# Performance work log

Measured on AMD Instinct MI355X. Metric: run time of the kernel, lower is better.

Reference implementation:

```python
import jax, jax.numpy as jnp
import numpy as np

D = 128      # hidden_dim
NH = 4       # nhead
FF = 64      # dim_feedforward
P = 16       # patch size
C, H, W = 3, 224, 224
NA = 15      # n_actions
BS = 256
NP = (H // P) * (W // P)      # 196 patches
PD = C * P * P                # 768 patch_dim


def _ln(x, s, b):
    m = jnp.mean(x, -1, keepdims=True)
    v = jnp.mean(jnp.square(x - m), -1, keepdims=True)
    return (x - m) / jnp.sqrt(v + 1e-5) * s + b


def _mha(q, k, v, Wqkv, bqkv, Wo, bo):
    # q,k,v: (L, B, D); Wqkv: (D, 3D) jax-layout; torch MultiheadAttention math
    Wq, Wk, Wv = jnp.split(Wqkv, 3, axis=1)
    bq, bk, bv = jnp.split(bqkv, 3)
    hd = D // NH
    Lq, B, _ = q.shape
    Lk = k.shape[0]
    Q = (q @ Wq + bq).reshape(Lq, B, NH, hd)
    K = (k @ Wk + bk).reshape(Lk, B, NH, hd)
    V = (v @ Wv + bv).reshape(Lk, B, NH, hd)
    scores = jnp.einsum('qbhd,kbhd->bhqk', Q, K) * np.float32(1.0 / np.sqrt(hd))
    attn = jax.nn.softmax(scores, axis=-1)
    out = jnp.einsum('bhqk,kbhd->qbhd', attn, V).reshape(Lq, B, D)
    return out @ Wo + bo


def setup_inputs() -> dict:
    key = jax.random.key(0)
    ks = iter(jax.random.split(key, 64))
    n = lambda shape, sc=0.02: (jax.random.normal(next(ks), shape, jnp.float32) * sc)
    inp = {
        'image': jax.random.normal(next(ks), (BS, C, H, W), jnp.float32),
        'angle': jax.random.normal(next(ks), (BS,), jnp.float32),
        'pos_x': jax.random.normal(next(ks), (BS,), jnp.float32),
        'pos_y': jax.random.normal(next(ks), (BS,), jnp.float32),
        'sk': jax.random.normal(next(ks), (BS, 200), jnp.float32),
        'patch_W': n((PD, D)), 'patch_b': n((D,)),
        'pos_emb': n((NP, 1, D), 1.0),
        'enc_qkv_W': n((D, 3 * D)), 'enc_qkv_b': n((3 * D,)),
        'enc_out_W': n((D, D)), 'enc_out_b': n((D,)),
        'enc_ln1_s': jnp.ones((D,)), 'enc_ln1_b': jnp.zeros((D,)),
        'enc_ff1_W': n((D, FF)), 'enc_ff1_b': n((FF,)),
        'enc_ff2_W': n((FF, D)), 'enc_ff2_b': n((D,)),
        'enc_ln2_s': jnp.ones((D,)), 'enc_ln2_b': jnp.zeros((D,)),
        'dec_sa_qkv_W': n((D, 3 * D)), 'dec_sa_qkv_b': n((3 * D,)),
        'dec_sa_out_W': n((D, D)), 'dec_sa_out_b': n((D,)),
        'dec_ca_qkv_W': n((D, 3 * D)), 'dec_ca_qkv_b': n((3 * D,)),
        'dec_ca_out_W': n((D, D)), 'dec_ca_out_b': n((D,)),
        'dec_ln1_s': jnp.ones((D,)), 'dec_ln1_b': jnp.zeros((D,)),
        'dec_ln2_s': jnp.ones((D,)), 'dec_ln2_b': jnp.zeros((D,)),
        'dec_ln3_s': jnp.ones((D,)), 'dec_ln3_b': jnp.zeros((D,)),
        'dec_ff1_W': n((D, FF)), 'dec_ff1_b': n((FF,)),
        'dec_ff2_W': n((FF, D)), 'dec_ff2_b': n((D,)),
        'dec_norm_s': jnp.ones((D,)), 'dec_norm_b': jnp.zeros((D,)),
        'sk1_W': n((200, 256)), 'sk1_b': n((256,)),
        'sk2_W': n((256, 256)), 'sk2_b': n((256,)),
        'sk3_W': n((256, 100)), 'sk3_b': n((100,)),
        'act_W': n((NA + 103, D)), 'act_b': n((D,)),
        'l1_W': n((D, D)), 'l1_b': n((D,)),
        'l2_W': n((D, 1)), 'l2_b': n((1,)),
    }
    return inp


def reference(image, angle, pos_x, pos_y, sk,
              patch_W, patch_b, pos_emb,
              enc_qkv_W, enc_qkv_b, enc_out_W, enc_out_b,
              enc_ln1_s, enc_ln1_b, enc_ff1_W, enc_ff1_b, enc_ff2_W, enc_ff2_b,
              enc_ln2_s, enc_ln2_b,
              dec_sa_qkv_W, dec_sa_qkv_b, dec_sa_out_W, dec_sa_out_b,
              dec_ca_qkv_W, dec_ca_qkv_b, dec_ca_out_W, dec_ca_out_b,
              dec_ln1_s, dec_ln1_b, dec_ln2_s, dec_ln2_b, dec_ln3_s, dec_ln3_b,
              dec_ff1_W, dec_ff1_b, dec_ff2_W, dec_ff2_b,
              dec_norm_s, dec_norm_b,
              sk1_W, sk1_b, sk2_W, sk2_b, sk3_W, sk3_b,
              act_W, act_b, l1_W, l1_b, l2_W, l2_b):
    b = image.shape[0]
    hh, ww = H // P, W // P
    # rearrange 'b c (h p1) (w p2) -> b (h w) (p1 p2 c)'
    x = image.reshape(b, C, hh, P, ww, P).transpose(0, 2, 4, 3, 5, 1).reshape(b, hh * ww, PD)
    src = (x @ patch_W + patch_b).transpose(1, 0, 2) + pos_emb  # (n, b, D)
    # encoder layer (post-norm, dropout=eval)
    s2 = _mha(src, src, src, enc_qkv_W, enc_qkv_b, enc_out_W, enc_out_b)
    src = _ln(src + s2, enc_ln1_s, enc_ln1_b)
    ff = jax.nn.relu(src @ enc_ff1_W + enc_ff1_b) @ enc_ff2_W + enc_ff2_b
    memory = _ln(src + ff, enc_ln2_s, enc_ln2_b)
    # sketch MLP
    s = jax.nn.relu(sk @ sk1_W + sk1_b)
    s = jax.nn.relu(s @ sk2_W + sk2_b)
    s = s @ sk3_W + sk3_b  # (b, 100)
    pos_ang = jnp.stack([angle, pos_x, pos_y], axis=1)  # (b, 3)
    # batched action encoding (replaces python double loop)
    nA = NA
    eye = jnp.broadcast_to(jnp.eye(nA, dtype=image.dtype)[None], (b, nA, nA))
    feats = jnp.concatenate([
        eye,
        jnp.broadcast_to(pos_ang[:, None, :], (b, nA, 3)),
        jnp.broadcast_to(s[:, None, :], (b, nA, 100)),
    ], axis=-1)  # (b, nA, nA+103)
    tgt = (feats @ act_W + act_b).transpose(1, 0, 2)  # (nA, b, D)
    # decoder layer (post-norm)
    t2 = _mha(tgt, tgt, tgt, dec_sa_qkv_W, dec_sa_qkv_b, dec_sa_out_W, dec_sa_out_b)
    tgt = _ln(tgt + t2, dec_ln1_s, dec_ln1_b)
    t2 = _mha(tgt, memory, memory, dec_ca_qkv_W, dec_ca_qkv_b, dec_ca_out_W, dec_ca_out_b)
    tgt = _ln(tgt + t2, dec_ln2_s, dec_ln2_b)
    ff = jax.nn.relu(tgt @ dec_ff1_W + dec_ff1_b) @ dec_ff2_W + dec_ff2_b
    tgt = _ln(tgt + ff, dec_ln3_s, dec_ln3_b)
    out = _ln(tgt, dec_norm_s, dec_norm_b)  # (nA, b, D)
    out = out.transpose(1, 0, 2)  # (b, nA, D)
    q = jax.nn.relu(out @ l1_W + l1_b) @ l2_W + l2_b  # (b, nA, 1)
    return q[..., 0]  # (b, nA)
```

## Files before the change

### kernel.cpp

```cpp
#include <hip/hip_runtime.h>
#include <math.h>

#define BSZ 256
#define DIM 128
#define NHD 4
#define NPATCH 196
#define NACT 15

typedef float f32x4 __attribute__((ext_vector_type(4)));
typedef __bf16 bf16x8 __attribute__((ext_vector_type(8)));
typedef short short8 __attribute__((ext_vector_type(8)));

__device__ __forceinline__ float wred_sum(float v) {
#pragma unroll
    for (int m = 1; m < 64; m <<= 1) v += __shfl_xor(v, m, 64);
    return v;
}
__device__ __forceinline__ float wred_max(float v) {
#pragma unroll
    for (int m = 1; m < 64; m <<= 1) v = fmaxf(v, __shfl_xor(v, m, 64));
    return v;
}
__device__ __forceinline__ ushort f2bf(float f) {
    unsigned u = __float_as_uint(f);
    return (ushort)((u + 0x7fffu + ((u >> 16) & 1u)) >> 16);
}

__global__ __launch_bounds__(256) void k_wconv(
    const float* __restrict__ pW, const float* __restrict__ qkvW,
    const float* __restrict__ outW, const float* __restrict__ ff1W,
    const float* __restrict__ ff2W, const float* __restrict__ ckvW,
    ushort* __restrict__ o)
{
    int i = blockIdx.x * 256 + threadIdx.x;
    if (i < 98304) {
        int n = i / 768, kp = i % 768;
        int c = kp >> 8, q = kp & 255;
        o[i] = f2bf(pW[(q * 3 + c) * 128 + n]); return;
    }
    i -= 98304;
    if (i < 49152) { int n = i >> 7, k = i & 127; o[98304 + i] = f2bf(qkvW[k * 384 + n]); return; }
    i -= 49152;
    if (i < 16384) { int n = i >> 7, k = i & 127; o[147456 + i] = f2bf(outW[k * 128 + n]); return; }
    i -= 16384;
    if (i < 8192)  { int n = i >> 7, k = i & 127; o[163840 + i] = f2bf(ff1W[k * 64 + n]); return; }
    i -= 8192;
    if (i < 8192)  { int n = i >> 6, k = i & 63;  o[172032 + i] = f2bf(ff2W[k * 128 + n]); return; }
    i -= 8192;
    if (i < 32768) { int n = i >> 7, k = i & 127; o[180224 + i] = f2bf(ckvW[k * 384 + 128 + n]); return; }
}

__global__ __launch_bounds__(512) void k_pg_dec1(
    const float* __restrict__ img, const ushort* __restrict__ Wt,
    const float* __restrict__ pbias, const float* __restrict__ pe,
    float* __restrict__ C, ushort* __restrict__ Cb,
    const float* __restrict__ sk,
    const float* __restrict__ W1, const float* __restrict__ b1,
    const float* __restrict__ W2, const float* __restrict__ b2,
    const float* __restrict__ W3, const float* __restrict__ b3,
    const float* __restrict__ ang, const float* __restrict__ px,
    const float* __restrict__ py,
    const float* __restrict__ actW, const float* __restrict__ actb,
    const float* __restrict__ saW, const float* __restrict__ sab,
    const float* __restrict__ saoW, const float* __restrict__ saob,
    const float* __restrict__ ln1s, const float* __restrict__ ln1b,
    const float* __restrict__ caW, const float* __restrict__ cab,
    float* __restrict__ TGo, float* __restrict__ DQ)
{
    extern __shared__ char smem[];
    const int t = threadIdx.x;
    const int w = t >> 6, l = t & 63;

    if (blockIdx.x >= 256) {
        ushort* As = (ushort*)smem;
        ushort* Ws = As + 2 * 64 * 64;
        const bool act = t < 256;
        const int pb = blockIdx.x - 256;
        const int p = pb >> 2, bq = pb & 3;
        const int hp_ = p / 14, wp = p % 14;
        const int r0 = p * 256 + bq * 64;
        const int wm = w >> 1, wn = w & 1;
        const int lrow = l & 15, lk = l >> 4;
        const int arow = (t & 255) >> 2;
        const int b_img = bq * 64 + arow;
        const float* gimg = img + (size_t)b_img * 150528 + hp_ * 3584 + wp * 16;

        f32x4 acc[2][4];
#pragma unroll
        for (int m = 0; m < 2; ++m)
#pragma unroll
            for (int n = 0; n < 4; ++n) acc[m][n] = (f32x4)0.f;

        float4 va[4];
        short8 wr[4];

        auto loadT = [&](int kc) {
            if (!act) return;
            const int c = kc >> 8, p1q = (kc >> 6) & 3;
            const float* gc = gimg + c * 50176 + p1q * 896;
#pragma unroll
            for (int i = 0; i < 4; ++i)
                va[i] = *(const float4*)(gc + i * 224 + (t & 3) * 4);
#pragma unroll
            for (int j = 0; j < 4; ++j) {
                const int i2 = t + 256 * j;
                const int row = i2 >> 3, ch = i2 & 7;
                wr[j] = *(const short8*)(Wt + (size_t)row * 768 + kc + ch * 8);
            }
        };
        auto storeT = [&](int buf) {
            if (!act) return;
            ushort* Ab = As + buf * 64 * 64;
            ushort* Wb = Ws + buf * 128 * 64;
#pragma unroll
            for (int i = 0; i < 4; ++i) {
                ushort4 o4;
                o4.x = f2bf(va[i].x); o4.y = f2bf(va[i].y);
                o4.z = f2bf(va[i].z); o4.w = f2bf(va[i].w);
                const int kq = (t & 3) + 4 * i;
                const int bo = (kq * 8) ^ ((arow & 7) << 4);
                *(ushort4*)((char*)Ab + arow * 128 + bo) = o4;
            }
#pragma unroll
            for (int j = 0; j < 4; ++j) {
                const int i2 = t + 256 * j;
                const int row = i2 >> 3, ch = i2 & 7;
                const int sw = (ch * 16) ^ ((row & 7) << 4);
                *(short8*)((char*)Wb + row * 128 + sw) = wr[j];
            }
        };
        auto mfmaT = [&](int buf) {
            if (!act) return;
            const ushort* Ab = As + buf * 64 * 64;
            const ushort* Wb = Ws + buf * 128 * 64;
#pragma unroll
            for (int ks = 0; ks < 2; ++ks) {
                bf16x8 af[2], bfr[4];
#pragma unroll
                for (int m = 0; m < 2; ++m) {
                    const int row = wm * 32 + m * 16 + lrow;
                    const int col = (ks * 64 + lk * 16) ^ ((row & 7) << 4);
                    af[m] = *(const bf16x8*)((const char*)Ab + row * 128 + col);
                }
#pragma unroll
                for (int n = 0; n < 4; ++n) {
                    const int row = wn * 64 + n * 16 + lrow;
                    const int col = (ks * 64 + lk * 16) ^ ((row & 7) << 4);
                    bfr[n] = *(const bf16x8*)((const char*)Wb + row * 128 + col);
                }
#pragma unroll
                for (int m = 0; m < 2; ++m)
#pragma unroll
                    for (int n = 0; n < 4; ++n)
                        acc[m][n] = __builtin_amdgcn_mfma_f32_16x16x32_bf16(
                            af[m], bfr[n], acc[m][n], 0, 0, 0);
            }
        };

        loadT(0);
        for (int it = 0; it < 12; it += 2) {
            storeT(0);
            if (it + 1 < 12) loadT((it + 1) * 64);
            __syncthreads();
            mfmaT(0);
            storeT(1);
            if (it + 2 < 12) loadT((it + 2) * 64);
            __syncthreads();
            mfmaT(1);
        }

        if (act) {
            const int crow0 = (l >> 4) * 4;
            const int ccol = l & 15;
#pragma unroll
            for (int m = 0; m < 2; ++m) {
                const int growb = r0 + wm * 32 + m * 16 + crow0;
#pragma unroll
                for (int n = 0; n < 4; ++n) {
                    const int gcol = wn * 64 + n * 16 + ccol;
                    const float bv = pbias[gcol] + pe[p * 128 + gcol];
#pragma unroll
                    for (int j = 0; j < 4; ++j) {
                        const int grow = growb + j;
                        const float v = acc[m][n][j] + bv;
                        C[(size_t)grow * 128 + gcol] = v;
                        Cb[(size_t)grow * 128 + gcol] = f2bf(v);
                    }
                }
            }
        }
        return;
    }

    float* tg  = (float*)smem;
    float* qkv = tg + 1920;
    float* ao  = qkv + 5820;
    float* xr  = ao + 1920;
    float* h1  = xr + 256;
    float* h2  = h1 + 256;
    float* s3  = h2 + 256;
    float* pbv = s3 + 100;
    float* hp  = pbv + 64;
    const int b = blockIdx.x;

    {
        float pf = 0.f;
#define PFW(P, N) for (int i = t * 32; i < (N); i += 512 * 32) pf += P[i];
        PFW(W1, 200 * 256)
        PFW(W2, 256 * 256)
        PFW(W3, 256 * 100)
        PFW(actW, 118 * 128)
        PFW(saW, 128 * 384)
        PFW(saoW, 128 * 128)
        PFW(caW, 128 * 384)
#undef PFW
        asm volatile("" :: "v"(pf));
    }

    if (t < 256) xr[t] = (t < 200) ? sk[(size_t)b * 200 + t] : 0.f;
    __syncthreads();
    {
        const int c = t & 255, g = t >> 8;
        const int k0 = g * 100;
        float a = 0.f;
#pragma unroll 10
        for (int k = k0; k < k0 + 100; ++k) a += xr[k] * W1[k * 256 + c];
        hp[g * 256 + c] = a;
    }
    __syncthreads();
    if (t < 256) h1[t] = fmaxf(hp[t] + hp[256 + t] + b1[t], 0.f);
    __syncthreads();
    {
        const int c = t & 255, g = t >> 8;
        const int k0 = g * 128;
        float a = 0.f;
#pragma unroll 8
        for (int k = k0; k < k0 + 128; ++k) a += h1[k] * W2[k * 256 + c];
        hp[g * 256 + c] = a;
    }
    __syncthreads();
    if (t < 256) h2[t] = fmaxf(hp[t] + hp[256 + t] + b2[t], 0.f);
    __syncthreads();
    if (t < 400) {
        const int c = t % 100, g = t / 100;
        const int k0 = g * 64;
        float a = 0.f;
#pragma unroll 8
        for (int k = k0; k < k0 + 64; ++k) a += h2[k] * W3[k * 100 + c];
        hp[g * 256 + c] = a;
    }
    __syncthreads();
    if (t < 100) s3[t] = hp[t] + hp[256 + t] + hp[512 + t] + hp[768 + t] + b3[t];
    __syncthreads();
    {
        const int c = t & 127, g = t >> 7;
        const int k0 = g * 25;
        float a = 0.f;
#pragma unroll 5
        for (int k = k0; k < k0 + 25; ++k) a += s3[k] * actW[(18 + k) * 128 + c];
        hp[g * 256 + c] = a;
    }
    __syncthreads();
    if (t < 128) {
        const float base = actb[t] + hp[t] + hp[256 + t] + hp[512 + t] + hp[768 + t] +
                           ang[b] * actW[15 * 128 + t] + px[b] * actW[16 * 128 + t] +
                           py[b] * actW[17 * 128 + t];
#pragma unroll
        for (int i = 0; i < 15; ++i) tg[i * 128 + t] = base + actW[i * 128 + t];
    }
    __syncthreads();

    if (t < 384) {
        float acc[15];
#pragma unroll
        for (int r = 0; r < 15; ++r) acc[r] = 0.f;
#pragma unroll 4
        for (int k = 0; k < 128; ++k) {
            const float wv = saW[(size_t)k * 384 + t];
#pragma unroll
            for (int r = 0; r < 15; ++r) acc[r] += tg[r * 128 + k] * wv;
        }
        const float bb = sab[t];
#pragma unroll
        for (int r = 0; r < 15; ++r) qkv[r * 388 + t] = acc[r] + bb;
    }
    __syncthreads();

    const float rs = 0.17677669529663687f;
    if (w < 4) {
        for (int qi = 0; qi < 15; ++qi) {
            float s = -3.0e38f;
            if (l < 15) {
                s = 0.f;
#pragma unroll
                for (int d = 0; d < 32; ++d)
                    s += qkv[qi * 388 + w * 32 + d] * qkv[l * 388 + 128 + w * 32 + d];
                s *= rs;
            }
            const float m = wred_max(s);
            const float pv = (l < 15) ? __expf(s - m) : 0.f;
            const float sum = wred_sum(pv);
            if (l < 15) pbv[w * 16 + l] = pv;
            if (l < 32) {
                float o = 0.f;
#pragma unroll
                for (int j = 0; j < 15; ++j) o += pbv[w * 16 + j] * qkv[j * 388 + 256 + w * 32 + l];
                ao[qi * 128 + w * 32 + l] = o / sum;
            }
        }
    }
    __syncthreads();

    {
        const int c = t & 127, g = t >> 7;
        const int r3 = (g + 12 < 15) ? g + 12 : 0;
        float a0 = 0.f, a1 = 0.f, a2 = 0.f, a3 = 0.f;
#pragma unroll 4
        for (int k = 0; k < 128; ++k) {
            const float wv = saoW[(size_t)k * 128 + c];
            a0 += ao[g * 128 + k] * wv;
            a1 += ao[(g + 4) * 128 + k] * wv;
            a2 += ao[(g + 8) * 128 + k] * wv;
            a3 += ao[r3 * 128 + k] * wv;
        }
        const float bb = saob[c];
        qkv[g * 388 + c]       = a0 + bb + tg[g * 128 + c];
        qkv[(g + 4) * 388 + c] = a1 + bb + tg[(g + 4) * 128 + c];
        qkv[(g + 8) * 388 + c] = a2 + bb + tg[(g + 8) * 128 + c];
        if (g + 12 < 15) qkv[(g + 12) * 388 + c] = a3 + bb + tg[(g + 12) * 128 + c];
    }
    __syncthreads();
    for (int r = w; r < 15; r += 8) {
        const float x0 = qkv[r * 388 + l], x1 = qkv[r * 388 + l + 64];
        const float sm = wred_sum(x0 + x1);
        const float sq = wred_sum(x0 * x0 + x1 * x1);
        const float mean = sm * 0.0078125f;
        const float rstd = rsqrtf(sq * 0.0078125f - mean * mean + 1e-5f);
        const float y0 = (x0 - mean) * rstd * ln1s[l] + ln1b[l];
        const float y1 = (x1 - mean) * rstd * ln1s[l + 64] + ln1b[l + 64];
        tg[r * 128 + l] = y0; tg[r * 128 + l + 64] = y1;
        float* g2 = TGo + ((size_t)r * 256 + b) * 128;
        g2[l] = y0; g2[l + 64] = y1;
    }
    __syncthreads();

    {
        const int c = t & 127, g = t >> 7;
        const int r3 = (g + 12 < 15) ? g + 12 : 0;
        float a0 = 0.f, a1 = 0.f, a2 = 0.f, a3 = 0.f;
#pragma unroll 4
        for (int k = 0; k < 128; ++k) {
            const float wv = caW[(size_t)k * 384 + c];
            a0 += tg[g * 128 + k] * wv;
            a1 += tg[(g + 4) * 128 + k] * wv;
            a2 += tg[(g + 8) * 128 + k] * wv;
            a3 += tg[r3 * 128 + k] * wv;
        }
        const float bb = cab[c];
        DQ[((size_t)g * 256 + b) * 128 + c]       = a0 + bb;
        DQ[((size_t)(g + 4) * 256 + b) * 128 + c] = a1 + bb;
        DQ[((size_t)(g + 8) * 256 + b) * 128 + c] = a2 + bb;
        if (g + 12 < 15) DQ[((size_t)(g + 12) * 256 + b) * 128 + c] = a3 + bb;
    }
}

template <int BM, int BN>
__global__ __launch_bounds__(256) void k_gemm_bf16(
    const ushort* __restrict__ A, int lda,
    const ushort* __restrict__ Wt, int K,
    const float* __restrict__ bias,
    float* __restrict__ C, ushort* __restrict__ Cb, int ldc,
    const float* __restrict__ pe, int relu)
{
    constexpr int NWN = BN / 64;
    constexpr int NWM = 4 / NWN;
    constexpr int WTM = BM / NWM;
    constexpr int MF = WTM / 16;
    __shared__ ushort As[BM * 64];
    __shared__ ushort Ws[BN * 64];
    const int t = threadIdx.x;
    const int w = t >> 6, l = t & 63;
    const int r0 = blockIdx.x * BM;
    const int n0 = blockIdx.y * BN;
    const int wm = w / NWN, wn = w % NWN;
    const int lrow = l & 15, lk = l >> 4;

    f32x4 acc[MF][4];
#pragma unroll
    for (int m = 0; m < MF; ++m)
#pragma unroll
        for (int n = 0; n < 4; ++n) acc[m][n] = (f32x4)0.f;

    for (int kc = 0; kc < K; kc += 64) {
        __syncthreads();
#pragma unroll
        for (int i = t; i < BM * 8; i += 256) {
            const int row = i >> 3, ch = i & 7;
            const int sw = (ch * 16) ^ ((row & 7) << 4);
            *(short8*)((char*)As + row * 128 + sw) =
                *(const short8*)(A + (size_t)(r0 + row) * lda + kc + ch * 8);
        }
#pragma unroll
        for (int i = t; i < BN * 8; i += 256) {
            const int row = i >> 3, ch = i & 7;
            const int sw = (ch * 16) ^ ((row & 7) << 4);
            *(short8*)((char*)Ws + row * 128 + sw) =
                *(const short8*)(Wt + (size_t)(n0 + row) * K + kc + ch * 8);
        }
        __syncthreads();
#pragma unroll
        for (int ks = 0; ks < 2; ++ks) {
            bf16x8 af[MF], bfr[4];
#pragma unroll
            for (int m = 0; m < MF; ++m) {
                const int row = wm * WTM + m * 16 + lrow;
                const int col = (ks * 64 + lk * 16) ^ ((row & 7) << 4);
                af[m] = *(const bf16x8*)((const char*)As + row * 128 + col);
            }
#pragma unroll
            for (int n = 0; n < 4; ++n) {
                const int row = wn * 64 + n * 16 + lrow;
                const int col = (ks * 64 + lk * 16) ^ ((row & 7) << 4);
                bfr[n] = *(const bf16x8*)((const char*)Ws + row * 128 + col);
            }
#pragma unroll
            for (int m = 0; m < MF; ++m)
#pragma unroll
                for (int n = 0; n < 4; ++n)
                    acc[m][n] = __builtin_amdgcn_mfma_f32_16x16x32_bf16(
                        af[m], bfr[n], acc[m][n], 0, 0, 0);
        }
    }

    const int crow0 = (l >> 4) * 4;
    const int ccol = l & 15;
#pragma unroll
    for (int m = 0; m < MF; ++m) {
        const int growb = r0 + wm * WTM + m * 16 + crow0;
#pragma unroll
        for (int n = 0; n < 4; ++n) {
            const int gcol = n0 + wn * 64 + n * 16 + ccol;
            const float bv = bias[gcol];
#pragma unroll
            for (int j = 0; j < 4; ++j) {
                const int grow = growb + j;
                float v = acc[m][n][j] + bv;
                if (pe) v += pe[(grow >> 8) * 128 + gcol];
                if (relu) v = fmaxf(v, 0.f);
                if (C)  C[(size_t)grow * ldc + gcol] = v;
                if (Cb) Cb[(size_t)grow * ldc + gcol] = f2bf(v);
            }
        }
    }
}

template <int FF>
__global__ __launch_bounds__(256) void k_gemm_ln(
    const ushort* __restrict__ A, int lda,
    const ushort* __restrict__ Wt, int K,
    const float* __restrict__ bias,
    const float* __restrict__ resid,
    const float* __restrict__ lns, const float* __restrict__ lnbi,
    float* __restrict__ Co, ushort* __restrict__ Cb,
    const ushort* __restrict__ ffW, const float* __restrict__ ffb,
    ushort* __restrict__ Fb)
{
    __shared__ ushort As[64 * 64];
    __shared__ ushort Ws[128 * 64];
    __shared__ float psum[64][2][2];
    __shared__ ushort ffWs[FF ? 64 * 128 : 2];
    const int t = threadIdx.x;
    const int w = t >> 6, l = t & 63;
    const int r0 = blockIdx.x * 64;
    const int wm = w >> 1, wn = w & 1;
    const int lrow = l & 15, lk = l >> 4;

    f32x4 acc[2][4];
#pragma unroll
    for (int m = 0; m < 2; ++m)
#pragma unroll
        for (int n = 0; n < 4; ++n) acc[m][n] = (f32x4)0.f;

    for (int kc = 0; kc < K; kc += 64) {
        __syncthreads();
#pragma unroll
        for (int i = t; i < 64 * 8; i += 256) {
            const int row = i >> 3, ch = i & 7;
            const int sw = (ch * 16) ^ ((row & 7) << 4);
            *(short8*)((char*)As + row * 128 + sw) =
                *(const short8*)(A + (size_t)(r0 + row) * lda + kc + ch * 8);
        }
#pragma unroll
        for (int i = t; i < 128 * 8; i += 256) {
            const int row = i >> 3, ch = i & 7;
            const int sw = (ch * 16) ^ ((row & 7) << 4);
            *(short8*)((char*)Ws + row * 128 + sw) =
                *(const short8*)(Wt + (size_t)row * K + kc + ch * 8);
        }
        __syncthreads();
#pragma unroll
        for (int ks = 0; ks < 2; ++ks) {
            bf16x8 af[2], bfr[4];
#pragma unroll
            for (int m = 0; m < 2; ++m) {
                const int row = wm * 32 + m * 16 + lrow;
                const int col = (ks * 64 + lk * 16) ^ ((row & 7) << 4);
                af[m] = *(const bf16x8*)((const char*)As + row * 128 + col);
            }
#pragma unroll
            for (int n = 0; n < 4; ++n) {
                const int row = wn * 64 + n * 16 + lrow;
                const int col = (ks * 64 + lk * 16) ^ ((row & 7) << 4);
                bfr[n] = *(const bf16x8*)((const char*)Ws + row * 128 + col);
            }
#pragma unroll
            for (int m = 0; m < 2; ++m)
#pragma unroll
                for (int n = 0; n < 4; ++n)
                    acc[m][n] = __builtin_amdgcn_mfma_f32_16x16x32_bf16(
                        af[m], bfr[n], acc[m][n], 0, 0, 0);
        }
    }

    const int crow0 = (l >> 4) * 4;
    const int ccol = l & 15;
#pragma unroll
    for (int m = 0; m < 2; ++m) {
        const int growb = r0 + wm * 32 + m * 16 + crow0;
#pragma unroll
        for (int n = 0; n < 4; ++n) {
            const int gcol = wn * 64 + n * 16 + ccol;
            const float bv = bias[gcol];
#pragma unroll
            for (int j = 0; j < 4; ++j) {
                float v = acc[m][n][j] + bv;
                if (resid) v += resid[(size_t)(growb + j) * 128 + gcol];
                acc[m][n][j] = v;
            }
        }
    }
#pragma unroll
    for (int m = 0; m < 2; ++m)
#pragma unroll
        for (int j = 0; j < 4; ++j) {
            float s_ = 0.f, q_ = 0.f;
#pragma unroll
            for (int n = 0; n < 4; ++n) {
                const float x = acc[m][n][j];
                s_ += x; q_ += x * x;
            }
#pragma unroll
            for (int mk = 1; mk < 16; mk <<= 1) {
                s_ += __shfl_xor(s_, mk, 64);
                q_ += __shfl_xor(q_, mk, 64);
            }
            if (ccol == 0) {
                const int r = wm * 32 + m * 16 + crow0 + j;
                psum[r][wn][0] = s_;
                psum[r][wn][1] = q_;
            }
        }
    __syncthreads();
    float mean_[2][4], rstd_[2][4];
#pragma unroll
    for (int m = 0; m < 2; ++m)
#pragma unroll
        for (int j = 0; j < 4; ++j) {
            const int r = wm * 32 + m * 16 + crow0 + j;
            const float sum = psum[r][0][0] + psum[r][1][0];
            const float sq  = psum[r][0][1] + psum[r][1][1];
            const float mean = sum * 0.0078125f;
            const float var = sq * 0.0078125f - mean * mean;
            mean_[m][j] = mean;
            rstd_[m][j] = rsqrtf(var + 1e-5f);
        }
#pragma unroll
    for (int m = 0; m < 2; ++m) {
        const int growb = r0 + wm * 32 + m * 16 + crow0;
#pragma unroll
        for (int n = 0; n < 4; ++n) {
            const int gcol = wn * 64 + n * 16 + ccol;
            const float sv = lns[gcol], bv2 = lnbi[gcol];
#pragma unroll
            for (int j = 0; j < 4; ++j) {
                const float y = (acc[m][n][j] - mean_[m][j]) * rstd_[m][j] * sv + bv2;
                acc[m][n][j] = y;
                const size_t oi = (size_t)(growb + j) * 128 + gcol;
                if (Co) Co[oi] = y;
                if (Cb) Cb[oi] = f2bf(y);
            }
        }
    }

    if constexpr (FF) {
#pragma unroll
        for (int m = 0; m < 2; ++m) {
            const int rowb = wm * 32 + m * 16 + crow0;
#pragma unroll
            for (int n = 0; n < 4; ++n) {
                const int c = wn * 64 + n * 16 + ccol;
                const int cb = ((c >> 3) * 16) ^ 0;
#pragma unroll
                for (int j = 0; j < 4; ++j) {
                    const int row = rowb + j;
                    const int bo = row * 256 + ((cb) ^ ((row & 7) << 4)) + (c & 7) * 2;
                    *(ushort*)((char*)Ws + bo) = f2bf(acc[m][n][j]);
                }
            }
        }
        for (int i = t; i < 1024; i += 256) {
            const int row = i >> 4, ch = i & 15;
            *(short8*)((char*)ffWs + row * 256 + ((ch * 16) ^ ((row & 7) << 4))) =
                *(const short8*)(ffW + (size_t)row * 128 + ch * 8);
        }
        __syncthreads();
        f32x4 accF[4];
#pragma unroll
        for (int n = 0; n < 4; ++n) accF[n] = (f32x4)0.f;
#pragma unroll
        for (int ks = 0; ks < 4; ++ks) {
            const int arow2 = w * 16 + lrow;
            const int acol = (ks * 64 + lk * 16) ^ ((arow2 & 7) << 4);
            const bf16x8 af = *(const bf16x8*)((const char*)Ws + arow2 * 256 + acol);
#pragma unroll
            for (int n = 0; n < 4; ++n) {
                const int brow = n * 16 + lrow;
                const int bcol = (ks * 64 + lk * 16) ^ ((brow & 7) << 4);
                const bf16x8 bf = *(const bf16x8*)((const char*)ffWs + brow * 256 + bcol);
                accF[n] = __builtin_amdgcn_mfma_f32_16x16x32_bf16(af, bf, accF[n], 0, 0, 0);
            }
        }
#pragma unroll
        for (int n = 0; n < 4; ++n) {
            const int gcol = n * 16 + ccol;
            const float bb = ffb[gcol];
#pragma unroll
            for (int j = 0; j < 4; ++j) {
                const int grow = r0 + w * 16 + crow0 + j;
                Fb[(size_t)grow * 64 + gcol] = f2bf(fmaxf(accF[n][j] + bb, 0.f));
            }
        }
    }
}

__global__ __launch_bounds__(256) void k_attn_mfma(
    const ushort* __restrict__ qkv, ushort* __restrict__ ob, float scale)
{
    __shared__ ushort Ks[208 * 40];
    __shared__ ushort Vt[32 * 232];
    __shared__ ushort Ps[4][16 * 232];
    const int bh = blockIdx.x;
    const int b = bh >> 2, h = bh & 3;
    const int t = threadIdx.x, w = t >> 6, l = t & 63;
    const int lr = l & 15, lg = l >> 4;

    for (int idx = t; idx < 784; idx += 256) {
        const int j = idx >> 2, ch = idx & 3;
        const size_t base = ((size_t)j * 256 + b) * 384 + h * 32 + ch * 8;
        *(short8*)(Ks + j * 40 + ch * 8) = *(const short8*)(qkv + base + 128);
        short8 v = *(const short8*)(qkv + base + 256);
#pragma unroll
        for (int q = 0; q < 8; ++q)
            Vt[(ch * 8 + q) * 232 + j] = (ushort)v[q];
    }
    for (int idx = t; idx < 32 * 36; idx += 256)
        Vt[(idx / 36) * 232 + 196 + (idx % 36)] = 0;
    for (int i = l; i < 256; i += 64)
        Ps[w][(i >> 4) * 232 + 208 + (i & 15)] = 0;
    __syncthreads();

    for (int qt = w; qt < 13; qt += 4) {
        int qr = qt * 16 + lr; if (qr > 195) qr = 195;
        const bf16x8 qf = *(const bf16x8*)(qkv + ((size_t)qr * 256 + b) * 384 + h * 32 + lg * 8);

        f32x4 s[13];
#pragma unroll
        for (int jn = 0; jn < 13; ++jn) {
            const bf16x8 kf = *(const bf16x8*)(Ks + (jn * 16 + lr) * 40 + lg * 8);
            s[jn] = __builtin_amdgcn_mfma_f32_16x16x32_bf16(qf, kf, (f32x4)0.f, 0, 0, 0);
        }
        if (lr >= 4) {
            s[12][0] = -3.0e38f; s[12][1] = -3.0e38f;
            s[12][2] = -3.0e38f; s[12][3] = -3.0e38f;
        }

        float inv[4];
        ushort* pw = Ps[w];
#pragma unroll
        for (int j = 0; j < 4; ++j) {
            float m = s[0][j];
#pragma unroll
            for (int jn = 1; jn < 13; ++jn) m = fmaxf(m, s[jn][j]);
            m = fmaxf(m, __shfl_xor(m, 1, 64));
            m = fmaxf(m, __shfl_xor(m, 2, 64));
            m = fmaxf(m, __shfl_xor(m, 4, 64));
            m = fmaxf(m, __shfl_xor(m, 8, 64));
            float sum = 0.f;
#pragma unroll
            for (int jn = 0; jn < 13; ++jn) {
                const float p = __expf((s[jn][j] - m) * scale);
                s[jn][j] = p;
                sum += p;
            }
            sum += __shfl_xor(sum, 1, 64);
            sum += __shfl_xor(sum, 2, 64);
            sum += __shfl_xor(sum, 4, 64);
            sum += __shfl_xor(sum, 8, 64);
            inv[j] = 1.0f / sum;
        }
#pragma unroll
        for (int jn = 0; jn < 13; ++jn)
#pragma unroll
            for (int j = 0; j < 4; ++j)
                pw[(lg * 4 + j) * 232 + jn * 16 + lr] = f2bf(s[jn][j]);

        f32x4 o0 = (f32x4)0.f, o1 = (f32x4)0.f;
#pragma unroll
        for (int kt = 0; kt < 7; ++kt) {
            const bf16x8 pf = *(const bf16x8*)(pw + lr * 232 + kt * 32 + lg * 8);
            const bf16x8 v0 = *(const bf16x8*)(Vt + lr * 232 + kt * 32 + lg * 8);
            const bf16x8 v1 = *(const bf16x8*)(Vt + (16 + lr) * 232 + kt * 32 + lg * 8);
            o0 = __builtin_amdgcn_mfma_f32_16x16x32_bf16(pf, v0, o0, 0, 0, 0);
            o1 = __builtin_amdgcn_mfma_f32_16x16x32_bf16(pf, v1, o1, 0, 0, 0);
        }
#pragma unroll
        for (int j = 0; j < 4; ++j) {
            const int r = qt * 16 + lg * 4 + j;
            if (r < 196) {
                const size_t o = ((size_t)r * 256 + b) * 128 + h * 32;
                ob[o + lr]      = f2bf(o0[j] * inv[j]);
                ob[o + 16 + lr] = f2bf(o1[j] * inv[j]);
            }
        }
    }
}

__global__ __launch_bounds__(256) void k_attn(
    const float* __restrict__ qp, int qstride,
    const float* __restrict__ kvp, int kvstride, int koff, int voff,
    float* __restrict__ op, ushort* __restrict__ ob,
    int Lq, int Lk, float scale)
{
    __shared__ float Kl[196 * 36];
    __shared__ float Vl[196 * 32];
    __shared__ float pbuf[4][256];
    const int bh = blockIdx.x;
    const int b = bh >> 2;
    const int h = bh & 3;
    const int t = threadIdx.x;
    const int w = t >> 6;
    const int l = t & 63;

    for (int idx = t; idx < Lk * 8; idx += 256) {
        const int j = idx >> 3;
        const int kq = idx & 7;
        const size_t row = ((size_t)j * 256 + b) * kvstride + h * 32 + kq * 4;
        *(float4*)(&Kl[j * 36 + kq * 4]) = *(const float4*)(kvp + row + koff);
        *(float4*)(&Vl[j * 32 + kq * 4]) = *(const float4*)(kvp + row + voff);
    }
    if ((Lk & 1) && t < 8) *(float4*)(&Vl[Lk * 32 + t * 4]) = make_float4(0.f, 0.f, 0.f, 0.f);
    __syncthreads();

    const int Lh = (Lk + 1) >> 1;
    const int half = l >> 5;
    const int kk = l & 31;
    const int jb = half * Lh;

    for (int jq = w; jq < Lq; jq += 4) {
        const float* qrow = qp + ((size_t)jq * 256 + b) * qstride + h * 32;
        float4 q4[8];
#pragma unroll
        for (int kq = 0; kq < 8; ++kq) q4[kq] = *(const float4*)(qrow + kq * 4);

        float s[4];
#pragma unroll
        for (int r = 0; r < 4; ++r) {
            const int j = l + (r << 6);
            float acc = -3.0e38f;
            if (j < Lk) {
                acc = 0.f;
#pragma unroll
                for (int kq = 0; kq < 8; ++kq) {
                    const float4 kv = *(const float4*)(&Kl[j * 36 + kq * 4]);
                    acc += q4[kq].x * kv.x + q4[kq].y * kv.y +
                           q4[kq].z * kv.z + q4[kq].w * kv.w;
                }
                acc *= scale;
            }
            s[r] = acc;
        }
        float m = fmaxf(fmaxf(s[0], s[1]), fmaxf(s[2], s[3]));
        m = wred_max(m);
        float sum = 0.f;
#pragma unroll
        for (int r = 0; r < 4; ++r) {
            const int j = l + (r << 6);
            float p = __expf(s[r] - m);
            if (j >= Lk) p = 0.f;
            pbuf[w][j] = p;
            sum += p;
        }
        sum = wred_sum(sum);
        const float inv = 1.0f / sum;
        __threadfence_block();

        float o = 0.f;
        for (int jj = 0; jj < Lh; ++jj) {
            const float pv = pbuf[w][jb + jj];
            const float vv = Vl[(jb + jj) * 32 + kk];
            o += pv * vv;
        }
        o += __shfl_xor(o, 32, 64);
        o *= inv;
        if (l < 32) {
            const size_t oi = ((size_t)jq * 256 + b) * 128 + h * 32 + l;
            if (op) op[oi] = o;
            if (ob) ob[oi] = f2bf(o);
        }
        __threadfence_block();
    }
}

__global__ __launch_bounds__(512) void k_dec2(
    const float* __restrict__ TGo, const float* __restrict__ AT,
    const float* __restrict__ caoW, const float* __restrict__ caob,
    const float* __restrict__ ln2s, const float* __restrict__ ln2b,
    const float* __restrict__ ff1W, const float* __restrict__ ff1b,
    const float* __restrict__ ff2W, const float* __restrict__ ff2b,
    const float* __restrict__ ln3s, const float* __restrict__ ln3b,
    const float* __restrict__ ns, const float* __restrict__ nb,
    const float* __restrict__ l1W, const float* __restrict__ l1b,
    const float* __restrict__ l2w, const float* __restrict__ l2b,
    float* __restrict__ qout)
{
    __shared__ float tg[15][128], ao[15][128], o2[15][128];
    __shared__ float ff[15][64];
    const int b = blockIdx.x, t = threadIdx.x;
    const int w = t >> 6, l = t & 63;

    {
        float pf = 0.f;
#define PFW(P, N) for (int i = t * 32; i < (N); i += 512 * 32) pf += P[i];
        PFW(caoW, 128 * 128)
        PFW(ff1W, 128 * 64)
        PFW(ff2W, 64 * 128)
        PFW(l1W, 128 * 128)
#undef PFW
        asm volatile("" :: "v"(pf));
    }

    for (int idx = t; idx < 1920; idx += 512) {
        const int r = idx >> 7, c = idx & 127;
        tg[r][c] = TGo[((size_t)r * 256 + b) * 128 + c];
        ao[r][c] = AT[((size_t)r * 256 + b) * 128 + c];
    }
    __syncthreads();

    {
        const int c = t & 127, g = t >> 7;
        const int r3 = (g + 12 < 15) ? g + 12 : 0;
        float a0 = 0.f, a1 = 0.f, a2 = 0.f, a3 = 0.f;
#pragma unroll 4
        for (int k = 0; k < 128; ++k) {
            const float wv = caoW[(size_t)k * 128 + c];
            a0 += ao[g][k] * wv;
            a1 += ao[g + 4][k] * wv;
            a2 += ao[g + 8][k] * wv;
            a3 += ao[r3][k] * wv;
        }
        const float bb = caob[c];
        o2[g][c]     = a0 + bb + tg[g][c];
        o2[g + 4][c] = a1 + bb + tg[g + 4][c];
        o2[g + 8][c] = a2 + bb + tg[g + 8][c];
        if (g + 12 < 15) o2[g + 12][c] = a3 + bb + tg[g + 12][c];
    }
    __syncthreads();
    for (int r = w; r < 15; r += 8) {
        const float x0 = o2[r][l], x1 = o2[r][l + 64];
        const float sm = wred_sum(x0 + x1);
        const float sq = wred_sum(x0 * x0 + x1 * x1);
        const float mean = sm * 0.0078125f;
        const float rstd = rsqrtf(sq * 0.0078125f - mean * mean + 1e-5f);
        tg[r][l]      = (x0 - mean) * rstd * ln2s[l] + ln2b[l];
        tg[r][l + 64] = (x1 - mean) * rstd * ln2s[l + 64] + ln2b[l + 64];
    }
    __syncthreads();
    {
        const int n = t & 63, g = t >> 6;
        const int r1 = (g + 8 < 15) ? g + 8 : 0;
        float a0 = 0.f, a1 = 0.f;
#pragma unroll 4
        for (int k = 0; k < 128; ++k) {
            const float wv = ff1W[(size_t)k * 64 + n];
            a0 += tg[g][k] * wv;
            a1 += tg[r1][k] * wv;
        }
        const float bb = ff1b[n];
        ff[g][n] = fmaxf(a0 + bb, 0.f);
        if (g + 8 < 15) ff[g + 8][n] = fmaxf(a1 + bb, 0.f);
    }
    __syncthreads();
    {
        const int c = t & 127, g = t >> 7;
        const int r3 = (g + 12 < 15) ? g + 12 : 0;
        float a0 = 0.f, a1 = 0.f, a2 = 0.f, a3 = 0.f;
#pragma unroll 4
        for (int k = 0; k < 64; ++k) {
            const float wv = ff2W[(size_t)k * 128 + c];
            a0 += ff[g][k] * wv;
            a1 += ff[g + 4][k] * wv;
            a2 += ff[g + 8][k] * wv;
            a3 += ff[r3][k] * wv;
        }
        const float bb = ff2b[c];
        o2[g][c]     = a0 + bb + tg[g][c];
        o2[g + 4][c] = a1 + bb + tg[g + 4][c];
        o2[g + 8][c] = a2 + bb + tg[g + 8][c];
        if (g + 12 < 15) o2[g + 12][c] = a3 + bb + tg[g + 12][c];
    }
    __syncthreads();
    for (int r = w; r < 15; r += 8) {
        const float x0 = o2[r][l], x1 = o2[r][l + 64];
        const float sm = wred_sum(x0 + x1);
        const float sq = wred_sum(x0 * x0 + x1 * x1);
        const float mean = sm * 0.0078125f;
        const float rstd = rsqrtf(sq * 0.0078125f - mean * mean + 1e-5f);
        const float y0 = (x0 - mean) * rstd * ln3s[l] + ln3b[l];
        const float y1 = (x1 - mean) * rstd * ln3s[l + 64] + ln3b[l + 64];
        const float sm2 = wred_sum(y0 + y1);
        const float sq2 = wred_sum(y0 * y0 + y1 * y1);
        const float mean2 = sm2 * 0.0078125f;
        const float rstd2 = rsqrtf(sq2 * 0.0078125f - mean2 * mean2 + 1e-5f);
        tg[r][l]      = (y0 - mean2) * rstd2 * ns[l] + nb[l];
        tg[r][l + 64] = (y1 - mean2) * rstd2 * ns[l + 64] + nb[l + 64];
    }
    __syncthreads();
    {
        const int c = t & 127, g = t >> 7;
        const int r3 = (g + 12 < 15) ? g + 12 : 0;
        float a0 = 0.f, a1 = 0.f, a2 = 0.f, a3 = 0.f;
#pragma unroll 4
        for (int k = 0; k < 128; ++k) {
            const float wv = l1W[(size_t)k * 128 + c];
            a0 += tg[g][k] * wv;
            a1 += tg[g + 4][k] * wv;
            a2 += tg[g + 8][k] * wv;
            a3 += tg[r3][k] * wv;
        }
        const float bb = l1b[c];
        o2[g][c]     = fmaxf(a0 + bb, 0.f);
        o2[g + 4][c] = fmaxf(a1 + bb, 0.f);
        o2[g + 8][c] = fmaxf(a2 + bb, 0.f);
        if (g + 12 < 15) o2[g + 12][c] = fmaxf(a3 + bb, 0.f);
    }
    __syncthreads();
    for (int r = w; r < 15; r += 8) {
        const float d = wred_sum(o2[r][l] * l2w[l] + o2[r][l + 64] * l2w[l + 64]);
        if (l == 0) qout[b * 15 + r] = d + l2b[0];
    }
}

extern "C" void kernel_launch(void* const* d_in, const int* in_sizes, int n_in,
                              void* d_out, int out_size, void* d_ws, size_t ws_size,
                              hipStream_t stream)
{
    (void)in_sizes; (void)n_in; (void)out_size; (void)ws_size;
    const float* image      = (const float*)d_in[0];
    const float* angle      = (const float*)d_in[1];
    const float* pos_x      = (const float*)d_in[2];
    const float* pos_y      = (const float*)d_in[3];
    const float* sk         = (const float*)d_in[4];
    const float* patch_W    = (const float*)d_in[5];
    const float* patch_b    = (const float*)d_in[6];
    const float* pos_emb    = (const float*)d_in[7];
    const float* enc_qkv_W  = (const float*)d_in[8];
    const float* enc_qkv_b  = (const float*)d_in[9];
    const float* enc_out_W  = (const float*)d_in[10];
    const float* enc_out_b  = (const float*)d_in[11];
    const float* enc_ln1_s  = (const float*)d_in[12];
    const float* enc_ln1_b  = (const float*)d_in[13];
    const float* enc_ff1_W  = (const float*)d_in[14];
    const float* enc_ff1_b  = (const float*)d_in[15];
    const float* enc_ff2_W  = (const float*)d_in[16];
    const float* enc_ff2_b  = (const float*)d_in[17];
    const float* enc_ln2_s  = (const float*)d_in[18];
    const float* enc_ln2_b  = (const float*)d_in[19];
    const float* dec_sa_qkv_W = (const float*)d_in[20];
    const float* dec_sa_qkv_b = (const float*)d_in[21];
    const float* dec_sa_out_W = (const float*)d_in[22];
    const float* dec_sa_out_b = (const float*)d_in[23];
    const float* dec_ca_qkv_W = (const float*)d_in[24];
    const float* dec_ca_qkv_b = (const float*)d_in[25];
    const float* dec_ca_out_W = (const float*)d_in[26];
    const float* dec_ca_out_b = (const float*)d_in[27];
    const float* dec_ln1_s  = (const float*)d_in[28];
    const float* dec_ln1_b  = (const float*)d_in[29];
    const float* dec_ln2_s  = (const float*)d_in[30];
    const float* dec_ln2_b  = (const float*)d_in[31];
    const float* dec_ln3_s  = (const float*)d_in[32];
    const float* dec_ln3_b  = (const float*)d_in[33];
    const float* dec_ff1_W  = (const float*)d_in[34];
    const float* dec_ff1_b  = (const float*)d_in[35];
    const float* dec_ff2_W  = (const float*)d_in[36];
    const float* dec_ff2_b  = (const float*)d_in[37];
    const float* dec_norm_s = (const float*)d_in[38];
    const float* dec_norm_b = (const float*)d_in[39];
    const float* sk1_W = (const float*)d_in[40];
    const float* sk1_b = (const float*)d_in[41];
    const float* sk2_W = (const float*)d_in[42];
    const float* sk2_b = (const float*)d_in[43];
    const float* sk3_W = (const float*)d_in[44];
    const float* sk3_b = (const float*)d_in[45];
    const float* act_W = (const float*)d_in[46];
    const float* act_b = (const float*)d_in[47];
    const float* l1_W  = (const float*)d_in[48];
    const float* l1_b  = (const float*)d_in[49];
    const float* l2_W  = (const float*)d_in[50];
    const float* l2_b  = (const float*)d_in[51];

    float* ws = (float*)d_ws;
    float* S0   = ws;
    float* QKVr = ws + 6422528;
    float* T0   = ws + 25690112;
    float* T1   = ws + 32112640;
    float* F1   = ws + 38535168;
    float* M0r  = ws + 41746432;
    float* S1s  = ws + 48168960;
    float* TG   = S1s + 156672;
    ushort* WTS = (ushort*)(ws + 48817152);

    ushort* QKVb = (ushort*)QKVr;
    float*  KV   = QKVr;
    float* DQ   = QKVr + 14319616;
    float* DT0  = T0;
    ushort* srcb = (ushort*)M0r;
    ushort* T0b  = (ushort*)M0r;
    ushort* F1b  = (ushort*)F1;
    ushort* M0b  = (ushort*)T1;
    ushort* wt_patch = WTS;
    ushort* wt_qkv   = WTS + 98304;
    ushort* wt_out   = WTS + 147456;
    ushort* wt_ff1   = WTS + 163840;
    ushort* wt_ff2   = WTS + 172032;
    ushort* wt_ckv   = WTS + 180224;

    const float rs = 0.17677669529663687f;

    k_wconv<<<dim3(832), 256, 0, stream>>>(patch_W, enc_qkv_W, enc_out_W,
                                           enc_ff1_W, enc_ff2_W, dec_ca_qkv_W, WTS);

    k_pg_dec1<<<dim3(1040), 512, 49152, stream>>>(
        image, wt_patch, patch_b, pos_emb, S0, srcb,
        sk, sk1_W, sk1_b, sk2_W, sk2_b, sk3_W, sk3_b,
        angle, pos_x, pos_y, act_W, act_b,
        dec_sa_qkv_W, dec_sa_qkv_b, dec_sa_out_W, dec_sa_out_b,
        dec_ln1_s, dec_ln1_b, dec_ca_qkv_W, dec_ca_qkv_b, TG, DQ);

    k_gemm_bf16<128, 128><<<dim3(392, 3), 256, 0, stream>>>(
        srcb, 128, wt_qkv, 128, enc_qkv_b, nullptr, QKVb, 384, nullptr, 0);
    k_attn_mfma<<<dim3(1024), 256, 0, stream>>>(QKVb, T0b, rs);
    k_gemm_ln<1><<<dim3(784), 256, 0, stream>>>(
        T0b, 128, wt_out, 128, enc_out_b, S0, enc_ln1_s, enc_ln1_b, S0, nullptr,
        wt_ff1, enc_ff1_b, F1b);
    k_gemm_ln<0><<<dim3(784), 256, 0, stream>>>(
        F1b, 64, wt_ff2, 64, enc_ff2_b, S0, enc_ln2_s, enc_ln2_b, nullptr, M0b,
        nullptr, nullptr, nullptr);
    k_gemm_bf16<128, 128><<<dim3(392, 2), 256, 0, stream>>>(
        M0b, 128, wt_ckv, 128, dec_ca_qkv_b + 128, KV, nullptr, 256, nullptr, 0);

    k_attn<<<dim3(1024), 256, 0, stream>>>(DQ, 128, KV, 256, 0, 128,
                                           DT0, nullptr, 15, 196, rs);
    k_dec2<<<dim3(256), 512, 0, stream>>>(
        TG, DT0, dec_ca_out_W, dec_ca_out_b, dec_ln2_s, dec_ln2_b,
        dec_ff1_W, dec_ff1_b, dec_ff2_W, dec_ff2_b,
        dec_ln3_s, dec_ln3_b, dec_norm_s, dec_norm_b,
        l1_W, l1_b, l2_W, l2_b, (float*)d_out);
}
```

Baseline: 313.6 us.

## Fuse encoder QKV projection into patch-embedding GEMM epilogue

The patch-embedding blocks now write their bf16 output tile into shared memory instead of global memory. They then compute the encoder QKV projection directly, loading the transposed QKV weights in three 128-column chunks into swizzled LDS. This removes the separate QKV GEMM launch and the global round trip of the bf16 source activations. In exchange, each patch block does extra serialized MFMA work with more barriers, which lengthens the first kernel.

```diff
diff --git a/kernel.cpp b/kernel.cpp
--- a/kernel.cpp
+++ b/kernel.cpp
@@ -53,7 +53,9 @@
 __global__ __launch_bounds__(512) void k_pg_dec1(
     const float* __restrict__ img, const ushort* __restrict__ Wt,
     const float* __restrict__ pbias, const float* __restrict__ pe,
-    float* __restrict__ C, ushort* __restrict__ Cb,
+    float* __restrict__ C,
+    const ushort* __restrict__ qkvWt, const float* __restrict__ qkvB,
+    ushort* __restrict__ QKVb,
     const float* __restrict__ sk,
     const float* __restrict__ W1, const float* __restrict__ b1,
     const float* __restrict__ W2, const float* __restrict__ b2,
@@ -169,23 +171,63 @@
             mfmaT(1);
         }
 
+        __syncthreads();
+        const int crow0 = (l >> 4) * 4;
+        const int ccol = l & 15;
         if (act) {
-            const int crow0 = (l >> 4) * 4;
-            const int ccol = l & 15;
 #pragma unroll
             for (int m = 0; m < 2; ++m) {
-                const int growb = r0 + wm * 32 + m * 16 + crow0;
+                const int rowb = wm * 32 + m * 16 + crow0;
 #pragma unroll
                 for (int n = 0; n < 4; ++n) {
-                    const int gcol = wn * 64 + n * 16 + ccol;
-                    const float bv = pbias[gcol] + pe[p * 128 + gcol];
+                    const int col = wn * 64 + n * 16 + ccol;
+                    const float bv = pbias[col] + pe[p * 128 + col];
 #pragma unroll
                     for (int j = 0; j < 4; ++j) {
-                        const int grow = growb + j;
+                        const int row = rowb + j;
                         const float v = acc[m][n][j] + bv;
-                        C[(size_t)grow * 128 + gcol] = v;
-                        Cb[(size_t)grow * 128 + gcol] = f2bf(v);
+                        C[(size_t)(r0 + row) * 128 + col] = v;
+                        const int bo = row * 256 + (((col >> 3) * 16) ^ ((row & 7) << 4)) + (col & 7) * 2;
+                        *(ushort*)((char*)As + bo) = f2bf(v);
                     }
+                }
+            }
+        }
+
+        const int wm2 = w >> 1;
+        const int wn2 = w & 1;
+        for (int cc = 0; cc < 3; ++cc) {
+            __syncthreads();
+            for (int i = t; i < 2048; i += 512) {
+                const int row = i >> 4, ch = i & 15;
+                *(short8*)((char*)Ws + row * 256 + ((ch * 16) ^ ((row & 7) << 4))) =
+                    *(const short8*)(qkvWt + (size_t)(cc * 128 + row) * 128 + ch * 8);
+            }
+            __syncthreads();
+            f32x4 a2[4];
+#pragma unroll
+            for (int n = 0; n < 4; ++n) a2[n] = (f32x4)0.f;
+#pragma unroll
+            for (int ks = 0; ks < 4; ++ks) {
+                const int arow2 = wm2 * 16 + lrow;
+                const int acol = (ks * 64 + lk * 16) ^ ((arow2 & 7) << 4);
+                const bf16x8 af = *(const bf16x8*)((const char*)As + arow2 * 256 + acol);
+#pragma unroll
+                for (int n = 0; n < 4; ++n) {
+                    const int brow = wn2 * 64 + n * 16 + lrow;
+                    const int bcol = (ks * 64 + lk * 16) ^ ((brow & 7) << 4);
+                    const bf16x8 bf = *(const bf16x8*)((const char*)Ws + brow * 256 + bcol);
+                    a2[n] = __builtin_amdgcn_mfma_f32_16x16x32_bf16(af, bf, a2[n], 0, 0, 0);
+                }
+            }
+#pragma unroll
+            for (int n = 0; n < 4; ++n) {
+                const int gcol = cc * 128 + wn2 * 64 + n * 16 + ccol;
+                const float bb = qkvB[gcol];
+#pragma unroll
+                for (int j = 0; j < 4; ++j) {
+                    const int grow = r0 + wm2 * 16 + crow0 + j;
+                    QKVb[(size_t)grow * 384 + gcol] = f2bf(a2[n][j] + bb);
                 }
             }
         }
@@ -1033,7 +1075,6 @@
     float*  KV   = QKVr;
     float* DQ   = QKVr + 14319616;
     float* DT0  = T0;
-    ushort* srcb = (ushort*)M0r;
     ushort* T0b  = (ushort*)M0r;
     ushort* F1b  = (ushort*)F1;
     ushort* M0b  = (ushort*)T1;
@@ -1050,14 +1091,13 @@
                                            enc_ff1_W, enc_ff2_W, dec_ca_qkv_W, WTS);
 
     k_pg_dec1<<<dim3(1040), 512, 49152, stream>>>(
-        image, wt_patch, patch_b, pos_emb, S0, srcb,
+        image, wt_patch, patch_b, pos_emb, S0,
+        wt_qkv, enc_qkv_b, QKVb,
         sk, sk1_W, sk1_b, sk2_W, sk2_b, sk3_W, sk3_b,
         angle, pos_x, pos_y, act_W, act_b,
         dec_sa_qkv_W, dec_sa_qkv_b, dec_sa_out_W, dec_sa_out_b,
         dec_ln1_s, dec_ln1_b, dec_ca_qkv_W, dec_ca_qkv_b, TG, DQ);
 
-    k_gemm_bf16<128, 128><<<dim3(392, 3), 256, 0, stream>>>(
-        srcb, 128, wt_qkv, 128, enc_qkv_b, nullptr, QKVb, 384, nullptr, 0);
     k_attn_mfma<<<dim3(1024), 256, 0, stream>>>(QKVb, T0b, rs);
     k_gemm_ln<1><<<dim3(784), 256, 0, stream>>>(
         T0b, 128, wt_out, 128, enc_out_b, S0, enc_ln1_s, enc_ln1_b, S0, nullptr,
```

New measurement: 294.2 us. 1.07x faster.
